# Kernel optimization log

Hardware: AMD Instinct MI355X
Metric: run time of the kernel (lower is better)

## Reference

```python
import jax, jax.numpy as jnp
import numpy as np

T, A = 10, 9           # input_dim_h, input_dim_w
HID = 128              # EncoderMLP hidden_dim default
D = 512                # n_latent_dims
G, K = 4, 32           # vqvae_groups, vqvae_n_embed
ACT_SCALE = 1.0


def setup_inputs() -> dict:
    key = jax.random.key(0)
    ks = jax.random.split(key, 16)
    N = 131072
    s = lambda k, shp, fan: jax.random.normal(k, shp, jnp.float32) * (1.0 / np.sqrt(fan))
    inp = {
        "state": jax.random.normal(ks[0], (N, T, A), jnp.float32),
        # encoder: (T*A)->128 relu, 128->128 relu, 128->512
        "enc_w1": s(ks[1], (T * A, HID), T * A), "enc_b1": jnp.zeros((HID,), jnp.float32),
        "enc_w2": s(ks[2], (HID, HID), HID),     "enc_b2": jnp.zeros((HID,), jnp.float32),
        "enc_w3": s(ks[3], (HID, D), HID),       "enc_b3": jnp.zeros((D,), jnp.float32),
        # decoder: 512->128 relu, 128->128 relu, 128->(T*A)
        "dec_w1": s(ks[4], (D, HID), D),         "dec_b1": jnp.zeros((HID,), jnp.float32),
        "dec_w2": s(ks[5], (HID, HID), HID),     "dec_b2": jnp.zeros((HID,), jnp.float32),
        "dec_w3": s(ks[6], (HID, T * A), HID),   "dec_b3": jnp.zeros((T * A,), jnp.float32),
        # residual VQ codebooks [G, K, D]
        "codebooks": jax.random.normal(ks[7], (G, K, D), jnp.float32),
    }
    return inp


def _mlp(x, w1, b1, w2, b2, w3, b3):
    h = jax.nn.relu(x @ w1 + b1)
    h = jax.nn.relu(h @ w2 + b2)
    return h @ w3 + b3


def reference(state, enc_w1, enc_b1, enc_w2, enc_b2, enc_w3, enc_b3,
              dec_w1, dec_b1, dec_w2, dec_b2, dec_w3, dec_b3, codebooks):
    N = state.shape[0]
    x = (state / ACT_SCALE).reshape(N, T * A)            # preprocess: 'N T A -> N (T A)'
    z = _mlp(x, enc_w1, enc_b1, enc_w2, enc_b2, enc_w3, enc_b3)  # [N, D]

    # Residual VQ over G quantizers (eval path): nearest-code per residual,
    # straight-through accumulation, per-quantizer commitment loss.
    residual = z
    quant = jnp.zeros_like(z)
    codes, losses = [], []
    for g in range(G):
        e = codebooks[g]                                  # [K, D]
        # ||r - e||^2 = ||r||^2 - 2 r.e + ||e||^2 ; ||r||^2 constant over K
        dist = jnp.sum(e * e, axis=-1)[None, :] - 2.0 * (residual @ e.T)  # [N, K]
        idx = jnp.argmin(dist, axis=-1)                   # [N]
        q = e[idx]                                        # [N, D] gather
        losses.append(jnp.mean((jax.lax.stop_gradient(q) - residual) ** 2))
        quant = quant + residual + jax.lax.stop_gradient(q - residual)  # straight-through
        residual = residual - jax.lax.stop_gradient(q)
        codes.append(idx)
    vq_code = jnp.stack(codes, axis=-1)                   # [N, G]
    vq_loss = jnp.sum(jnp.stack(losses))

    recon = _mlp(quant, dec_w1, dec_b1, dec_w2, dec_b2, dec_w3, dec_b3) * ACT_SCALE
    recon = recon.reshape(N, T, A)                        # 'N (T A) -> N T A'
    return quant, vq_code, recon, vq_loss
```

## Files before the change

kernel.cpp:

```cpp
#include <hip/hip_runtime.h>
#include <hip/hip_bf16.h>

#define NSAMP 131072
#define TA    90
#define HID   128
#define DLAT  512

#define OFF_CODE  67108864ll
#define OFF_RECON (67108864ll + 524288ll)
#define OFF_LOSS  (67108864ll + 524288ll + 11796480ll)

#define PZF    8704
#define SHF    8960
#define MSKF   8256
#define H2AF   8272
#define H2BF   8400
#define TAU    0.08f

typedef __attribute__((ext_vector_type(8))) short bf16x8;
typedef __attribute__((ext_vector_type(4))) short s16x4;
typedef __attribute__((ext_vector_type(4))) float f32x4;
typedef unsigned short ushort_t;
#define MFMA16(a, b, c) __builtin_amdgcn_mfma_f32_16x16x32_bf16(a, b, c, 0, 0, 0)

__device__ __forceinline__ ushort_t f2bf(float f) {
    unsigned u = __float_as_uint(f);
    u = (u + 0x7FFF + ((u >> 16) & 1)) >> 16;
    return (ushort_t)u;
}
__device__ __forceinline__ float bf2f(ushort_t u) {
    return __uint_as_float(((unsigned)u) << 16);
}

__device__ __forceinline__ float dot512(const float* __restrict__ a,
                                        const float* __restrict__ b) {
    float s = 0.f;
    for (int i = 0; i < 128; ++i) {
        float4 x = ((const float4*)a)[i], y = ((const float4*)b)[i];
        s += x.x * y.x + x.y * y.y + x.z * y.z + x.w * y.w;
    }
    return s;
}

__global__ void k_prep(const float* __restrict__ cb, const float* __restrict__ w3,
                       const float* __restrict__ b3, const float* __restrict__ w1d,
                       const float* __restrict__ w2d, const float* __restrict__ w3d,
                       const float* __restrict__ w2e, const float* __restrict__ w1e,
                       float* __restrict__ P, float* __restrict__ M,
                       float* __restrict__ t0, float* __restrict__ v,
                       float* __restrict__ csc, float* __restrict__ cbW,
                       ushort_t* __restrict__ Qbf, ushort_t* __restrict__ w2bf,
                       ushort_t* __restrict__ w3bf,
                       ushort_t* __restrict__ Mhibf, ushort_t* __restrict__ Mlobf,
                       ushort_t* __restrict__ w2ehi, ushort_t* __restrict__ w2elo,
                       ushort_t* __restrict__ w1ehi, ushort_t* __restrict__ w1elo) {
    int tbl = blockIdx.x >> 6;
    int gid = (blockIdx.x & 63) * 256 + threadIdx.x;
    int i = gid >> 7, j = gid & 127;
    if (tbl == 0) {
        P[gid] = dot512(cb + (size_t)i * 512, cb + (size_t)j * 512);
        if (gid < 128) t0[gid] = dot512(cb + (size_t)gid * 512, b3);
        if (gid == 0) csc[0] = dot512(b3, b3);
    } else if (tbl == 1) {
        M[gid] = dot512(w3 + (size_t)i * 512, cb + (size_t)j * 512);
    } else if (tbl == 2) {
        Qbf[gid] = f2bf(dot512(w3 + (size_t)i * 512, w3 + (size_t)j * 512));
        if (gid < 128) v[gid] = dot512(w3 + (size_t)gid * 512, b3);
    } else if (tbl == 3) {
        float s = 0.f;
        for (int d = 0; d < 512; ++d) s = fmaf(cb[(size_t)i * 512 + d], w1d[d * 128 + j], s);
        cbW[gid] = s;
    } else if (tbl == 4) {
        w2bf[gid] = f2bf(w2d[j * 128 + i]);
    } else if (tbl == 5) {
        if (gid < 96 * 128)
            w3bf[gid] = (i < 90) ? f2bf(w3d[j * TA + i]) : (ushort_t)0;
    } else if (tbl == 6) {
        float d = dot512(w3 + (size_t)j * 512, cb + (size_t)i * 512);
        ushort_t hi = f2bf(d);
        Mhibf[gid] = hi;
        Mlobf[gid] = f2bf(d - bf2f(hi));
    } else if (tbl == 7) {
        float d = w2e[j * 128 + i];
        ushort_t hi = f2bf(d);
        w2ehi[gid] = hi;
        w2elo[gid] = f2bf(d - bf2f(hi));
    } else {
        float d = (j < 90) ? w1e[(size_t)j * 128 + i] : 0.f;
        ushort_t hi = f2bf(d);
        w1ehi[gid] = hi;
        w1elo[gid] = f2bf(d - bf2f(hi));
    }
}

__launch_bounds__(256, 4)
__global__ void k_encvq(const float* __restrict__ X,
                        const float* __restrict__ w1, const float* __restrict__ b1,
                        const float* __restrict__ w2, const float* __restrict__ b2,
                        const ushort_t* __restrict__ w1ehi, const ushort_t* __restrict__ w1elo,
                        const ushort_t* __restrict__ w2ehi, const ushort_t* __restrict__ w2elo,
                        const float* __restrict__ Mt, const ushort_t* __restrict__ Qbf,
                        const ushort_t* __restrict__ Mhi, const ushort_t* __restrict__ Mlo,
                        const float* __restrict__ t0g, const float* __restrict__ vg,
                        const float* __restrict__ cg, const float* __restrict__ Pg,
                        float* __restrict__ codes_out, float* __restrict__ loss_acc) {
    __shared__ __align__(16) float SH[SHF];
    ushort_t* sphi = (ushort_t*)SH;
    ushort_t* splo = (ushort_t*)(SH + 4096);
    const int t = threadIdx.x;
    const int row0 = blockIdx.x * 64;
    const int wv = t >> 6, lane = t & 63, lr = lane & 15, lg = lane >> 4;

    for (int it = 0; it < 24; ++it) {
        int idx = it * 256 + t;
        int s = idx / 96, j = idx - 96 * s;
        float xv = (j < 90) ? X[(size_t)(row0 + s) * TA + j] : 0.f;
        ushort_t hi = f2bf(xv);
        int adr = ((s << 7) + j) ^ ((s & 7) << 3);
        sphi[adr] = hi;
        splo[adr] = f2bf(xv - bf2f(hi));
    }
    __syncthreads();

    {
        f32x4 c1[2][4];
#pragma unroll
        for (int m = 0; m < 2; ++m)
#pragma unroll
            for (int n = 0; n < 4; ++n) c1[m][n] = (f32x4){0.f, 0.f, 0.f, 0.f};
#pragma unroll
        for (int kt = 0; kt < 3; ++kt) {
            bf16x8 ah[2], al[2], bhi[4], blo[4];
#pragma unroll
            for (int m = 0; m < 2; ++m) {
                int arow = (32 * wv + 16 * m + lr) * 128 + kt * 32 + lg * 8;
                ah[m] = *(const bf16x8*)&w1ehi[arow];
                al[m] = *(const bf16x8*)&w1elo[arow];
            }
#pragma unroll
            for (int n = 0; n < 4; ++n) {
                int s = 16 * n + lr;
                int adr = ((s << 7) + kt * 32 + lg * 8) ^ ((s & 7) << 3);
                bhi[n] = *(const bf16x8*)&sphi[adr];
                blo[n] = *(const bf16x8*)&splo[adr];
            }
#pragma unroll
            for (int m = 0; m < 2; ++m)
#pragma unroll
                for (int n = 0; n < 4; ++n) {
                    c1[m][n] = MFMA16(ah[m], bhi[n], c1[m][n]);
                    c1[m][n] = MFMA16(ah[m], blo[n], c1[m][n]);
                    c1[m][n] = MFMA16(al[m], bhi[n], c1[m][n]);
                }
        }
        __syncthreads();
        float rbf[2][4];
#pragma unroll
        for (int m = 0; m < 2; ++m)
#pragma unroll
            for (int r = 0; r < 4; ++r) rbf[m][r] = b1[32 * wv + 16 * m + lg * 4 + r];
#pragma unroll
        for (int m = 0; m < 2; ++m)
#pragma unroll
            for (int n = 0; n < 4; ++n) {
                int s = 16 * n + lr;
                s16x4 ph, pl;
#pragma unroll
                for (int r = 0; r < 4; ++r) {
                    float hv = fmaxf(c1[m][n][r] + rbf[m][r], 0.f);
                    ushort_t hi = f2bf(hv);
                    ph[r] = (short)hi;
                    pl[r] = (short)f2bf(hv - bf2f(hi));
                }
                int ob2 = 32 * wv + 16 * m + lg * 4;
                int adr = ((s << 7) + ob2) ^ ((s & 7) << 3);
                *(s16x4*)&sphi[adr] = ph;
                *(s16x4*)&splo[adr] = pl;
            }
    }
    __syncthreads();

    {
        f32x4 c2[2][4];
#pragma unroll
        for (int m = 0; m < 2; ++m)
#pragma unroll
            for (int n = 0; n < 4; ++n) c2[m][n] = (f32x4){0.f, 0.f, 0.f, 0.f};
#pragma unroll
        for (int kt = 0; kt < 4; ++kt) {
            bf16x8 ah[2], al[2], bhi[4], blo[4];
#pragma unroll
            for (int m = 0; m < 2; ++m) {
                int arow = (32 * wv + 16 * m + lr) * 128 + kt * 32 + lg * 8;
                ah[m] = *(const bf16x8*)&w2ehi[arow];
                al[m] = *(const bf16x8*)&w2elo[arow];
            }
#pragma unroll
            for (int n = 0; n < 4; ++n) {
                int s = 16 * n + lr;
                int adr = ((s << 7) + kt * 32 + lg * 8) ^ ((s & 7) << 3);
                bhi[n] = *(const bf16x8*)&sphi[adr];
                blo[n] = *(const bf16x8*)&splo[adr];
            }
#pragma unroll
            for (int m = 0; m < 2; ++m)
#pragma unroll
                for (int n = 0; n < 4; ++n) {
                    c2[m][n] = MFMA16(ah[m], bhi[n], c2[m][n]);
                    c2[m][n] = MFMA16(ah[m], blo[n], c2[m][n]);
                    c2[m][n] = MFMA16(al[m], bhi[n], c2[m][n]);
                }
        }
        __syncthreads();
        float rbf[2][4];
#pragma unroll
        for (int m = 0; m < 2; ++m)
#pragma unroll
            for (int r = 0; r < 4; ++r) rbf[m][r] = b2[32 * wv + 16 * m + lg * 4 + r];
#pragma unroll
        for (int m = 0; m < 2; ++m)
#pragma unroll
            for (int n = 0; n < 4; ++n) {
                int s = 16 * n + lr;
                s16x4 ph, pl;
#pragma unroll
                for (int r = 0; r < 4; ++r) {
                    float hv = fmaxf(c2[m][n][r] + rbf[m][r], 0.f);
                    ushort_t hi = f2bf(hv);
                    ph[r] = (short)hi;
                    pl[r] = (short)f2bf(hv - bf2f(hi));
                }
                int ob2 = 32 * wv + 16 * m + lg * 4;
                int adr = ((s << 7) + ob2) ^ ((s & 7) << 3);
                *(s16x4*)&sphi[adr] = ph;
                *(s16x4*)&splo[adr] = pl;
            }
    }
    __syncthreads();

    f32x4 sc[2][4];
    {
        f32x4 qc[2][4];
#pragma unroll
        for (int m = 0; m < 2; ++m)
#pragma unroll
            for (int n = 0; n < 4; ++n) {
                qc[m][n] = (f32x4){0.f, 0.f, 0.f, 0.f};
                sc[m][n] = (f32x4){0.f, 0.f, 0.f, 0.f};
            }
#pragma unroll
        for (int kt = 0; kt < 4; ++kt) {
            bf16x8 aq[2], amh[2], aml[2], bhi[4], blo[4];
#pragma unroll
            for (int m = 0; m < 2; ++m) {
                int arow = (32 * wv + 16 * m + lr) * 128 + kt * 32 + lg * 8;
                aq[m]  = *(const bf16x8*)&Qbf[arow];
                amh[m] = *(const bf16x8*)&Mhi[arow];
                aml[m] = *(const bf16x8*)&Mlo[arow];
            }
#pragma unroll
            for (int n = 0; n < 4; ++n) {
                int s = 16 * n + lr;
                int adr = ((s << 7) + kt * 32 + lg * 8) ^ ((s & 7) << 3);
                bhi[n] = *(const bf16x8*)&sphi[adr];
                blo[n] = *(const bf16x8*)&splo[adr];
            }
#pragma unroll
            for (int m = 0; m < 2; ++m)
#pragma unroll
                for (int n = 0; n < 4; ++n) {
                    qc[m][n] = MFMA16(aq[m], bhi[n], qc[m][n]);
                    sc[m][n] = MFMA16(amh[m], bhi[n], sc[m][n]);
                    sc[m][n] = MFMA16(amh[m], blo[n], sc[m][n]);
                    sc[m][n] = MFMA16(aml[m], bhi[n], sc[m][n]);
                }
        }
        float v2[2][4];
#pragma unroll
        for (int m = 0; m < 2; ++m)
#pragma unroll
            for (int r = 0; r < 4; ++r) v2[m][r] = 2.f * vg[32 * wv + 16 * m + lg * 4 + r];
#pragma unroll
        for (int n = 0; n < 4; ++n) {
            int s = 16 * n + lr;
            float p = 0.f;
#pragma unroll
            for (int m = 0; m < 2; ++m)
#pragma unroll
                for (int r = 0; r < 4; ++r) {
                    int o = 32 * wv + 16 * m + lg * 4 + r;
                    int adr = ((s << 7) + o) ^ ((s & 7) << 3);
                    float hv = bf2f(sphi[adr]) + bf2f(splo[adr]);
                    p = fmaf(qc[m][n][r] + v2[m][r], hv, p);
                }
            p += __shfl_xor(p, 16);
            p += __shfl_xor(p, 32);
            if (lg == 0) SH[PZF + wv * 64 + s] = p;
        }
    }
    __syncthreads();

#pragma unroll
    for (int m = 0; m < 2; ++m)
#pragma unroll
        for (int n = 0; n < 4; ++n) {
            int s = 16 * n + lr;
#pragma unroll
            for (int r = 0; r < 4; ++r) {
                int o = 32 * wv + 16 * m + lg * 4 + r;
                SH[s * 129 + o] = sc[m][n][r] + t0g[o];
            }
        }
    __syncthreads();

    int cs[4];
    if (t < 64) {
        float marg = 3.4e38f;
#pragma unroll
        for (int g = 0; g < 4; ++g) {
            float best = 3.4e38f, best2 = 3.4e38f; int bi = g * 32;
#pragma unroll
            for (int k = 0; k < 32; ++k) {
                int c = g * 32 + k;
                float zd = SH[t * 129 + c];
                float nr = Pg[c * 128 + c];
                float a2 = 0.f;
#pragma unroll
                for (int gp = 0; gp < g; ++gp) a2 += Pg[cs[gp] * 128 + c];
                float dist = nr - 2.f * (zd - a2);
                if (dist < best) { best2 = best; best = dist; bi = c; }
                else if (dist < best2) { best2 = dist; }
            }
            cs[g] = bi;
            float m2 = best2 - best;
            marg = (m2 < marg) ? m2 : marg;
        }
        unsigned long long mk = __ballot(marg < TAU);
        if (t == 0) *(unsigned long long*)&SH[MSKF] = mk;
    }
    __syncthreads();

    const unsigned long long mask = *(const unsigned long long*)&SH[MSKF];

    {
        unsigned long long mk = mask;
        while (mk) {
            int nA = (int)__ffsll((long long)mk) - 1; mk &= mk - 1;
            int nB = -1;
            if (mk) { nB = (int)__ffsll((long long)mk) - 1; mk &= mk - 1; }
            int grp = t >> 7, tt = t & 127;
            int s2 = grp ? nB : nA;
            float hv1 = 0.f;
            if (s2 >= 0) {
                const float* xr = X + (size_t)(row0 + s2) * TA;
                for (int j = 0; j < 90; ++j)
                    hv1 = fmaf(xr[j], w1[j * 128 + tt], hv1);
                hv1 = fmaxf(hv1 + b1[tt], 0.f);
                SH[(grp ? H2BF : H2AF) + tt] = hv1;
            }
            __syncthreads();
            float hv2 = 0.f;
            if (s2 >= 0) {
                const float* h1c = &SH[grp ? H2BF : H2AF];
                for (int j = 0; j < 128; ++j)
                    hv2 = fmaf(h1c[j], w2[(size_t)j * 128 + tt], hv2);
                hv2 = fmaxf(hv2 + b2[tt], 0.f);
            }
            __syncthreads();
            if (s2 >= 0) SH[(grp ? H2BF : H2AF) + tt] = hv2;
            __syncthreads();
            if (s2 >= 0) {
                const float* h2c = &SH[grp ? H2BF : H2AF];
                float a = 0.f;
                for (int j = 0; j < 128; ++j)
                    a = fmaf(h2c[j], Mt[(size_t)j * 128 + tt], a);
                SH[s2 * 129 + tt] = a + t0g[tt];
            }
            __syncthreads();
        }
    }

    if (t < 64 && ((mask >> t) & 1ull)) {
#pragma unroll
        for (int g = 0; g < 4; ++g) {
            float best = 3.4e38f; int bi = g * 32;
#pragma unroll
            for (int k = 0; k < 32; ++k) {
                int c = g * 32 + k;
                float zd = SH[t * 129 + c];
                float nr = Pg[c * 128 + c];
                float a2 = 0.f;
#pragma unroll
                for (int gp = 0; gp < g; ++gp) a2 += Pg[cs[gp] * 128 + c];
                float dist = nr - 2.f * (zd - a2);
                if (dist < best) { best = dist; bi = c; }
            }
            cs[g] = bi;
        }
    }

    if (t < 64) {
        float znorm = cg[0] + SH[PZF + t] + SH[PZF + 64 + t]
                    + SH[PZF + 128 + t] + SH[PZF + 192 + t];
        float S1 = 0.f, Sp = 0.f, msum = 0.f;
#pragma unroll
        for (int g = 0; g < 4; ++g) {
            int c = cs[g];
            float zd = SH[t * 129 + c];
            float nr = Pg[c * 128 + c];
            float a2 = 0.f;
#pragma unroll
            for (int gp = 0; gp < g; ++gp) a2 += Pg[cs[gp] * 128 + c];
            S1 += zd;
            Sp += nr + 2.f * a2;
            msum += (znorm - 2.f * S1 + Sp);
            codes_out[(size_t)(row0 + t) * 4 + g] = (float)(c - g * 32);
        }
#pragma unroll
        for (int off = 32; off; off >>= 1) msum += __shfl_down(msum, off);
        if (t == 0) atomicAdd(&loss_acc[0], msum);
    }
}

__launch_bounds__(256, 4)
__global__ void k_dec(const float* __restrict__ codes_f, const float* __restrict__ cb,
                      const float* __restrict__ cbW, const float* __restrict__ b1,
                      const ushort_t* __restrict__ w2bf, const float* __restrict__ b2,
                      const ushort_t* __restrict__ w3bf, const float* __restrict__ b3,
                      float* __restrict__ quant_out, float* __restrict__ recon_out) {
    __shared__ __align__(16) unsigned char SHB[39424];
    int* cods = (int*)SHB;
    ushort_t* h2bf = (ushort_t*)SHB;
    ushort_t* h1bf = (ushort_t*)(SHB + 16384);
    float* Rl = (float*)(SHB + 16384);
    const int t = threadIdx.x;
    const int st = t & 15, ct = t >> 4;
    const int s0 = st * 4, o0 = ct * 8;
    const int row0 = blockIdx.x * 64;

    cods[t] = ((t & 3) << 5) + (int)codes_f[(size_t)row0 * 4 + t];
    float rb1[8];
#pragma unroll
    for (int i = 0; i < 8; ++i) rb1[i] = b1[o0 + i];
    __syncthreads();

    for (int i = 0; i < 32; ++i) {
        int idx4 = i * 256 + t;
        int s = idx4 >> 7, d4 = (idx4 & 127) * 4;
        const int* cp = &cods[s * 4];
        float4 a = *(const float4*)&cb[(size_t)cp[0] * 512 + d4];
        float4 b = *(const float4*)&cb[(size_t)cp[1] * 512 + d4];
        float4 c = *(const float4*)&cb[(size_t)cp[2] * 512 + d4];
        float4 d = *(const float4*)&cb[(size_t)cp[3] * 512 + d4];
        float4 vv;
        vv.x = a.x + b.x + c.x + d.x;
        vv.y = a.y + b.y + c.y + d.y;
        vv.z = a.z + b.z + c.z + d.z;
        vv.w = a.w + b.w + c.w + d.w;
        *(float4*)&quant_out[(size_t)(row0 + s) * 512 + d4] = vv;
    }

    {
        float accL[8][4];
#pragma unroll
        for (int b = 0; b < 4; ++b) {
            const int* cp = &cods[(s0 + b) * 4];
            float u[8] = {0, 0, 0, 0, 0, 0, 0, 0};
#pragma unroll
            for (int g = 0; g < 4; ++g) {
                const float* r = &cbW[(size_t)cp[g] * 128 + o0];
                float4 x0 = *(const float4*)r, x1 = *(const float4*)(r + 4);
                u[0] += x0.x; u[1] += x0.y; u[2] += x0.z; u[3] += x0.w;
                u[4] += x1.x; u[5] += x1.y; u[6] += x1.z; u[7] += x1.w;
            }
#pragma unroll
            for (int a = 0; a < 8; ++a) accL[a][b] = u[a];
        }
#pragma unroll
        for (int b = 0; b < 4; ++b) {
            int s = s0 + b;
            bf16x8 pk;
#pragma unroll
            for (int a = 0; a < 8; ++a)
                pk[a] = (short)f2bf(fmaxf(accL[a][b] + rb1[a], 0.f));
            *(bf16x8*)&h1bf[((s << 7) + o0) ^ ((s & 7) << 3)] = pk;
        }
    }
    __syncthreads();

    const int wv = t >> 6, lane = t & 63, lr = lane & 15, lg = lane >> 4;

    {
        f32x4 c2[2][4];
#pragma unroll
        for (int m = 0; m < 2; ++m)
#pragma unroll
            for (int n = 0; n < 4; ++n) c2[m][n] = (f32x4){0.f, 0.f, 0.f, 0.f};
#pragma unroll
        for (int kt = 0; kt < 4; ++kt) {
            bf16x8 af[2], bfr[4];
#pragma unroll
            for (int m = 0; m < 2; ++m)
                af[m] = *(const bf16x8*)&w2bf[(32 * wv + 16 * m + lr) * 128 + kt * 32 + lg * 8];
#pragma unroll
            for (int n = 0; n < 4; ++n) {
                int s = 16 * n + lr;
                bfr[n] = *(const bf16x8*)&h1bf[((s << 7) + kt * 32 + lg * 8) ^ ((s & 7) << 3)];
            }
#pragma unroll
            for (int m = 0; m < 2; ++m)
#pragma unroll
                for (int n = 0; n < 4; ++n)
                    c2[m][n] = MFMA16(af[m], bfr[n], c2[m][n]);
        }
        float rb[2][4];
#pragma unroll
        for (int m = 0; m < 2; ++m)
#pragma unroll
            for (int r = 0; r < 4; ++r) rb[m][r] = b2[32 * wv + 16 * m + lg * 4 + r];
#pragma unroll
        for (int m = 0; m < 2; ++m)
#pragma unroll
            for (int n = 0; n < 4; ++n) {
                int s = 16 * n + lr;
                s16x4 pk;
#pragma unroll
                for (int r = 0; r < 4; ++r)
                    pk[r] = (short)f2bf(fmaxf(c2[m][n][r] + rb[m][r], 0.f));
                int ob2 = 32 * wv + 16 * m + lg * 4;
                *(s16x4*)&h2bf[((s << 7) + ob2) ^ ((s & 7) << 3)] = pk;
            }
    }
    __syncthreads();

    {
        f32x4 c3[6];
#pragma unroll
        for (int m = 0; m < 6; ++m) c3[m] = (f32x4){0.f, 0.f, 0.f, 0.f};
        const int sB = 16 * wv + lr;
#pragma unroll
        for (int kt = 0; kt < 4; ++kt) {
            bf16x8 bfr = *(const bf16x8*)&h2bf[((sB << 7) + kt * 32 + lg * 8) ^ ((sB & 7) << 3)];
#pragma unroll
            for (int mt = 0; mt < 6; ++mt) {
                bf16x8 af = *(const bf16x8*)&w3bf[(16 * mt + lr) * 128 + kt * 32 + lg * 8];
                c3[mt] = MFMA16(af, bfr, c3[mt]);
            }
        }
#pragma unroll
        for (int mt = 0; mt < 6; ++mt)
#pragma unroll
            for (int r = 0; r < 4; ++r) {
                int o = 16 * mt + lg * 4 + r;
                if (o < 90) Rl[sB * 90 + o] = c3[mt][r] + b3[o];
            }
    }
    __syncthreads();

    {
        const float4* R4v = (const float4*)Rl;
        float4* G4 = (float4*)(recon_out + (size_t)row0 * 90);
#pragma unroll
        for (int it = 0; it < 6; ++it) {
            int i4 = it * 256 + t;
            if (i4 < 1440) G4[i4] = R4v[i4];
        }
    }
}

__global__ void k_loss(const float* __restrict__ acc, float* __restrict__ out) {
    out[0] = acc[0] * (1.0f / ((float)NSAMP * (float)DLAT));
}

extern "C" void kernel_launch(void* const* d_in, const int* in_sizes, int n_in,
                              void* d_out, int out_size, void* d_ws, size_t ws_size,
                              hipStream_t stream) {
    const float* state  = (const float*)d_in[0];
    const float* enc_w1 = (const float*)d_in[1];
    const float* enc_b1 = (const float*)d_in[2];
    const float* enc_w2 = (const float*)d_in[3];
    const float* enc_b2 = (const float*)d_in[4];
    const float* enc_w3 = (const float*)d_in[5];
    const float* enc_b3 = (const float*)d_in[6];
    const float* dec_w1 = (const float*)d_in[7];
    const float* dec_b1 = (const float*)d_in[8];
    const float* dec_w2 = (const float*)d_in[9];
    const float* dec_b2 = (const float*)d_in[10];
    const float* dec_w3 = (const float*)d_in[11];
    const float* dec_b3 = (const float*)d_in[12];
    const float* cb     = (const float*)d_in[13];

    float* out = (float*)d_out;
    float* P   = out;
    float* M   = out + 16384;
    ushort_t* Mhi = (ushort_t*)(out + 32768);
    ushort_t* Mlo = (ushort_t*)(out + 40960);
    float* t0  = out + 49152;
    float* v   = out + 49280;
    float* csc = out + 49408;
    ushort_t* w2ehi = (ushort_t*)(out + 49664);
    ushort_t* w2elo = (ushort_t*)(out + 57856);
    ushort_t* w1ehi = (ushort_t*)(out + 66048);
    ushort_t* w1elo = (ushort_t*)(out + 74240);
    float* ws = (float*)d_ws;
    float* loss_acc = ws;
    float* cbW = ws + 256;
    ushort_t* Qbf  = (ushort_t*)(ws + 16640);
    ushort_t* w2bf = (ushort_t*)(ws + 24832);
    ushort_t* w3bf = (ushort_t*)(ws + 33024);

    hipMemsetAsync(d_ws, 0, 16, stream);
    k_prep<<<576, 256, 0, stream>>>(cb, enc_w3, enc_b3, dec_w1, dec_w2, dec_w3,
                                    enc_w2, enc_w1,
                                    P, M, t0, v, csc, cbW, Qbf, w2bf, w3bf,
                                    Mhi, Mlo, w2ehi, w2elo, w1ehi, w1elo);
    k_encvq<<<NSAMP / 64, 256, 0, stream>>>(state, enc_w1, enc_b1, enc_w2, enc_b2,
                                            w1ehi, w1elo, w2ehi, w2elo,
                                            M, Qbf, Mhi, Mlo, t0, v, csc, P,
                                            out + OFF_CODE, loss_acc);
    k_dec<<<NSAMP / 64, 256, 0, stream>>>(out + OFF_CODE, cb, cbW,
                                          dec_b1, w2bf, dec_b2, w3bf, dec_b3,
                                          out, out + OFF_RECON);
    k_loss<<<1, 1, 0, stream>>>(loss_acc, out + OFF_LOSS);
}
```

Before: 352.3 us.

## Fuse encoder-VQ and decoder into one kernel when workspace is large enough

```diff
diff --git a/kernel.cpp b/kernel.cpp
--- a/kernel.cpp
+++ b/kernel.cpp
@@ -30,6 +30,11 @@
 }
 __device__ __forceinline__ float bf2f(ushort_t u) {
     return __uint_as_float(((unsigned)u) << 16);
+}
+__device__ __forceinline__ void nt_store4(float* p, float x0, float x1,
+                                          float x2, float x3) {
+    f32x4 v = {x0, x1, x2, x3};
+    __builtin_nontemporal_store(v, (f32x4*)p);
 }
 
 __device__ __forceinline__ float dot512(const float* __restrict__ a,
@@ -93,6 +98,511 @@
     }
 }
 
+__device__ __forceinline__ void enc_body(
+        const float* __restrict__ X,
+        const float* __restrict__ ew1, const float* __restrict__ eb1,
+        const float* __restrict__ ew2, const float* __restrict__ eb2,
+        const ushort_t* __restrict__ w1ehi, const ushort_t* __restrict__ w1elo,
+        const ushort_t* __restrict__ w2ehi, const ushort_t* __restrict__ w2elo,
+        const float* __restrict__ Mt, const ushort_t* __restrict__ Qbf,
+        const ushort_t* __restrict__ Mhi, const ushort_t* __restrict__ Mlo,
+        const float* __restrict__ t0g, const float* __restrict__ vg,
+        const float* __restrict__ cg, const float* __restrict__ Pg,
+        float* __restrict__ codes_out, float* __restrict__ loss_acc,
+        float* SH, int t, int row0, int (&cs)[4]) {
+    ushort_t* sphi = (ushort_t*)SH;
+    ushort_t* splo = (ushort_t*)(SH + 4096);
+    const int wv = t >> 6, lane = t & 63, lr = lane & 15, lg = lane >> 4;
+
+    for (int it = 0; it < 24; ++it) {
+        int idx = it * 256 + t;
+        int s = idx / 96, j = idx - 96 * s;
+        float xv = (j < 90) ? X[(size_t)(row0 + s) * TA + j] : 0.f;
+        ushort_t hi = f2bf(xv);
+        int adr = ((s << 7) + j) ^ ((s & 7) << 3);
+        sphi[adr] = hi;
+        splo[adr] = f2bf(xv - bf2f(hi));
+    }
+    __syncthreads();
+
+    {
+        f32x4 c1[2][4];
+#pragma unroll
+        for (int m = 0; m < 2; ++m)
+#pragma unroll
+            for (int n = 0; n < 4; ++n) c1[m][n] = (f32x4){0.f, 0.f, 0.f, 0.f};
+#pragma unroll
+        for (int kt = 0; kt < 3; ++kt) {
+            bf16x8 ah[2], al[2], bhi[4], blo[4];
+#pragma unroll
+            for (int m = 0; m < 2; ++m) {
+                int arow = (32 * wv + 16 * m + lr) * 128 + kt * 32 + lg * 8;
+                ah[m] = *(const bf16x8*)&w1ehi[arow];
+                al[m] = *(const bf16x8*)&w1elo[arow];
+            }
+#pragma unroll
+            for (int n = 0; n < 4; ++n) {
+                int s = 16 * n + lr;
+                int adr = ((s << 7) + kt * 32 + lg * 8) ^ ((s & 7) << 3);
+                bhi[n] = *(const bf16x8*)&sphi[adr];
+                blo[n] = *(const bf16x8*)&splo[adr];
+            }
+#pragma unroll
+            for (int m = 0; m < 2; ++m)
+#pragma unroll
+                for (int n = 0; n < 4; ++n) {
+                    c1[m][n] = MFMA16(ah[m], bhi[n], c1[m][n]);
+                    c1[m][n] = MFMA16(ah[m], blo[n], c1[m][n]);
+                    c1[m][n] = MFMA16(al[m], bhi[n], c1[m][n]);
+                }
+        }
+        __syncthreads();
+        float rbf[2][4];
+#pragma unroll
+        for (int m = 0; m < 2; ++m)
+#pragma unroll
+            for (int r = 0; r < 4; ++r) rbf[m][r] = eb1[32 * wv + 16 * m + lg * 4 + r];
+#pragma unroll
+        for (int m = 0; m < 2; ++m)
+#pragma unroll
+            for (int n = 0; n < 4; ++n) {
+                int s = 16 * n + lr;
+                s16x4 ph, pl;
+#pragma unroll
+                for (int r = 0; r < 4; ++r) {
+                    float hv = fmaxf(c1[m][n][r] + rbf[m][r], 0.f);
+                    ushort_t hi = f2bf(hv);
+                    ph[r] = (short)hi;
+                    pl[r] = (short)f2bf(hv - bf2f(hi));
+                }
+                int ob2 = 32 * wv + 16 * m + lg * 4;
+                int adr = ((s << 7) + ob2) ^ ((s & 7) << 3);
+                *(s16x4*)&sphi[adr] = ph;
+                *(s16x4*)&splo[adr] = pl;
+            }
+    }
+    __syncthreads();
+
+    {
+        f32x4 c2[2][4];
+#pragma unroll
+        for (int m = 0; m < 2; ++m)
+#pragma unroll
+            for (int n = 0; n < 4; ++n) c2[m][n] = (f32x4){0.f, 0.f, 0.f, 0.f};
+#pragma unroll
+        for (int kt = 0; kt < 4; ++kt) {
+            bf16x8 ah[2], al[2], bhi[4], blo[4];
+#pragma unroll
+            for (int m = 0; m < 2; ++m) {
+                int arow = (32 * wv + 16 * m + lr) * 128 + kt * 32 + lg * 8;
+                ah[m] = *(const bf16x8*)&w2ehi[arow];
+                al[m] = *(const bf16x8*)&w2elo[arow];
+            }
+#pragma unroll
+            for (int n = 0; n < 4; ++n) {
+                int s = 16 * n + lr;
+                int adr = ((s << 7) + kt * 32 + lg * 8) ^ ((s & 7) << 3);
+                bhi[n] = *(const bf16x8*)&sphi[adr];
+                blo[n] = *(const bf16x8*)&splo[adr];
+            }
+#pragma unroll
+            for (int m = 0; m < 2; ++m)
+#pragma unroll
+                for (int n = 0; n < 4; ++n) {
+                    c2[m][n] = MFMA16(ah[m], bhi[n], c2[m][n]);
+                    c2[m][n] = MFMA16(ah[m], blo[n], c2[m][n]);
+                    c2[m][n] = MFMA16(al[m], bhi[n], c2[m][n]);
+                }
+        }
+        __syncthreads();
+        float rbf[2][4];
+#pragma unroll
+        for (int m = 0; m < 2; ++m)
+#pragma unroll
+            for (int r = 0; r < 4; ++r) rbf[m][r] = eb2[32 * wv + 16 * m + lg * 4 + r];
+#pragma unroll
+        for (int m = 0; m < 2; ++m)
+#pragma unroll
+            for (int n = 0; n < 4; ++n) {
+                int s = 16 * n + lr;
+                s16x4 ph, pl;
+#pragma unroll
+                for (int r = 0; r < 4; ++r) {
+                    float hv = fmaxf(c2[m][n][r] + rbf[m][r], 0.f);
+                    ushort_t hi = f2bf(hv);
+                    ph[r] = (short)hi;
+                    pl[r] = (short)f2bf(hv - bf2f(hi));
+                }
+                int ob2 = 32 * wv + 16 * m + lg * 4;
+                int adr = ((s << 7) + ob2) ^ ((s & 7) << 3);
+                *(s16x4*)&sphi[adr] = ph;
+                *(s16x4*)&splo[adr] = pl;
+            }
+    }
+    __syncthreads();
+
+    f32x4 sc[2][4];
+    {
+        f32x4 qc[2][4];
+#pragma unroll
+        for (int m = 0; m < 2; ++m)
+#pragma unroll
+            for (int n = 0; n < 4; ++n) {
+                qc[m][n] = (f32x4){0.f, 0.f, 0.f, 0.f};
+                sc[m][n] = (f32x4){0.f, 0.f, 0.f, 0.f};
+            }
+#pragma unroll
+        for (int kt = 0; kt < 4; ++kt) {
+            bf16x8 aq[2], amh[2], aml[2], bhi[4], blo[4];
+#pragma unroll
+            for (int m = 0; m < 2; ++m) {
+                int arow = (32 * wv + 16 * m + lr) * 128 + kt * 32 + lg * 8;
+                aq[m]  = *(const bf16x8*)&Qbf[arow];
+                amh[m] = *(const bf16x8*)&Mhi[arow];
+                aml[m] = *(const bf16x8*)&Mlo[arow];
+            }
+#pragma unroll
+            for (int n = 0; n < 4; ++n) {
+                int s = 16 * n + lr;
+                int adr = ((s << 7) + kt * 32 + lg * 8) ^ ((s & 7) << 3);
+                bhi[n] = *(const bf16x8*)&sphi[adr];
+                blo[n] = *(const bf16x8*)&splo[adr];
+            }
+#pragma unroll
+            for (int m = 0; m < 2; ++m)
+#pragma unroll
+                for (int n = 0; n < 4; ++n) {
+                    qc[m][n] = MFMA16(aq[m], bhi[n], qc[m][n]);
+                    sc[m][n] = MFMA16(amh[m], bhi[n], sc[m][n]);
+                    sc[m][n] = MFMA16(amh[m], blo[n], sc[m][n]);
+                    sc[m][n] = MFMA16(aml[m], bhi[n], sc[m][n]);
+                }
+        }
+        float v2[2][4];
+#pragma unroll
+        for (int m = 0; m < 2; ++m)
+#pragma unroll
+            for (int r = 0; r < 4; ++r) v2[m][r] = 2.f * vg[32 * wv + 16 * m + lg * 4 + r];
+#pragma unroll
+        for (int n = 0; n < 4; ++n) {
+            int s = 16 * n + lr;
+            float p = 0.f;
+#pragma unroll
+            for (int m = 0; m < 2; ++m)
+#pragma unroll
+                for (int r = 0; r < 4; ++r) {
+                    int o = 32 * wv + 16 * m + lg * 4 + r;
+                    int adr = ((s << 7) + o) ^ ((s & 7) << 3);
+                    float hv = bf2f(sphi[adr]) + bf2f(splo[adr]);
+                    p = fmaf(qc[m][n][r] + v2[m][r], hv, p);
+                }
+            p += __shfl_xor(p, 16);
+            p += __shfl_xor(p, 32);
+            if (lg == 0) SH[PZF + wv * 64 + s] = p;
+        }
+    }
+    __syncthreads();
+
+#pragma unroll
+    for (int m = 0; m < 2; ++m)
+#pragma unroll
+        for (int n = 0; n < 4; ++n) {
+            int s = 16 * n + lr;
+#pragma unroll
+            for (int r = 0; r < 4; ++r) {
+                int o = 32 * wv + 16 * m + lg * 4 + r;
+                SH[s * 129 + o] = sc[m][n][r] + t0g[o];
+            }
+        }
+    __syncthreads();
+
+    if (t < 64) {
+        float marg = 3.4e38f;
+#pragma unroll
+        for (int g = 0; g < 4; ++g) {
+            float best = 3.4e38f, best2 = 3.4e38f; int bi = g * 32;
+#pragma unroll
+            for (int k = 0; k < 32; ++k) {
+                int c = g * 32 + k;
+                float zd = SH[t * 129 + c];
+                float nr = Pg[c * 128 + c];
+                float a2 = 0.f;
+#pragma unroll
+                for (int gp = 0; gp < g; ++gp) a2 += Pg[cs[gp] * 128 + c];
+                float dist = nr - 2.f * (zd - a2);
+                if (dist < best) { best2 = best; best = dist; bi = c; }
+                else if (dist < best2) { best2 = dist; }
+            }
+            cs[g] = bi;
+            float m2 = best2 - best;
+            marg = (m2 < marg) ? m2 : marg;
+        }
+        unsigned long long mk = __ballot(marg < TAU);
+        if (t == 0) *(unsigned long long*)&SH[MSKF] = mk;
+    }
+    __syncthreads();
+
+    const unsigned long long mask = *(const unsigned long long*)&SH[MSKF];
+
+    {
+        unsigned long long mk = mask;
+        while (mk) {
+            int nA = (int)__ffsll((long long)mk) - 1; mk &= mk - 1;
+            int nB = -1;
+            if (mk) { nB = (int)__ffsll((long long)mk) - 1; mk &= mk - 1; }
+            int grp = t >> 7, tt = t & 127;
+            int s2 = grp ? nB : nA;
+            float hv1 = 0.f;
+            if (s2 >= 0) {
+                const float* xr = X + (size_t)(row0 + s2) * TA;
+                for (int j = 0; j < 90; ++j)
+                    hv1 = fmaf(xr[j], ew1[j * 128 + tt], hv1);
+                hv1 = fmaxf(hv1 + eb1[tt], 0.f);
+                SH[(grp ? H2BF : H2AF) + tt] = hv1;
+            }
+            __syncthreads();
+            float hv2 = 0.f;
+            if (s2 >= 0) {
+                const float* h1c = &SH[grp ? H2BF : H2AF];
+                for (int j = 0; j < 128; ++j)
+                    hv2 = fmaf(h1c[j], ew2[(size_t)j * 128 + tt], hv2);
+                hv2 = fmaxf(hv2 + eb2[tt], 0.f);
+            }
+            __syncthreads();
+            if (s2 >= 0) SH[(grp ? H2BF : H2AF) + tt] = hv2;
+            __syncthreads();
+            if (s2 >= 0) {
+                const float* h2c = &SH[grp ? H2BF : H2AF];
+                float a = 0.f;
+                for (int j = 0; j < 128; ++j)
+                    a = fmaf(h2c[j], Mt[(size_t)j * 128 + tt], a);
+                SH[s2 * 129 + tt] = a + t0g[tt];
+            }
+            __syncthreads();
+        }
+    }
+
+    if (t < 64 && ((mask >> t) & 1ull)) {
+#pragma unroll
+        for (int g = 0; g < 4; ++g) {
+            float best = 3.4e38f; int bi = g * 32;
+#pragma unroll
+            for (int k = 0; k < 32; ++k) {
+                int c = g * 32 + k;
+                float zd = SH[t * 129 + c];
+                float nr = Pg[c * 128 + c];
+                float a2 = 0.f;
+#pragma unroll
+                for (int gp = 0; gp < g; ++gp) a2 += Pg[cs[gp] * 128 + c];
+                float dist = nr - 2.f * (zd - a2);
+                if (dist < best) { best = dist; bi = c; }
+            }
+            cs[g] = bi;
+        }
+    }
+
+    if (t < 64) {
+        float znorm = cg[0] + SH[PZF + t] + SH[PZF + 64 + t]
+                    + SH[PZF + 128 + t] + SH[PZF + 192 + t];
+        float S1 = 0.f, Sp = 0.f, msum = 0.f;
+#pragma unroll
+        for (int g = 0; g < 4; ++g) {
+            int c = cs[g];
+            float zd = SH[t * 129 + c];
+            float nr = Pg[c * 128 + c];
+            float a2 = 0.f;
+#pragma unroll
+            for (int gp = 0; gp < g; ++gp) a2 += Pg[cs[gp] * 128 + c];
+            S1 += zd;
+            Sp += nr + 2.f * a2;
+            msum += (znorm - 2.f * S1 + Sp);
+            codes_out[(size_t)(row0 + t) * 4 + g] = (float)(cs[g] - g * 32);
+        }
+#pragma unroll
+        for (int off = 32; off; off >>= 1) msum += __shfl_down(msum, off);
+        if (t == 0) atomicAdd(&loss_acc[0], msum);
+    }
+}
+
+__device__ __forceinline__ void dec_body(
+        const float* __restrict__ cb, const float* __restrict__ cbW,
+        const float* __restrict__ b1, const ushort_t* __restrict__ w2bf,
+        const float* __restrict__ b2, const ushort_t* __restrict__ w3bf,
+        const float* __restrict__ b3,
+        float* __restrict__ quant_out, float* __restrict__ recon_out,
+        unsigned char* SHB, int t, int row0) {
+    int* cods = (int*)SHB;
+    ushort_t* h2bf = (ushort_t*)SHB;
+    ushort_t* h1bf = (ushort_t*)(SHB + 16384);
+    float* Rl = (float*)(SHB + 16384);
+    const int st = t & 15, ct = t >> 4;
+    const int s0 = st * 4, o0 = ct * 8;
+
+    float rb1[8];
+#pragma unroll
+    for (int i = 0; i < 8; ++i) rb1[i] = b1[o0 + i];
+
+    for (int i = 0; i < 32; ++i) {
+        int idx4 = i * 256 + t;
+        int s = idx4 >> 7, d4 = (idx4 & 127) * 4;
+        const int* cp = &cods[s * 4];
+        float4 a = *(const float4*)&cb[(size_t)cp[0] * 512 + d4];
+        float4 b = *(const float4*)&cb[(size_t)cp[1] * 512 + d4];
+        float4 c = *(const float4*)&cb[(size_t)cp[2] * 512 + d4];
+        float4 d = *(const float4*)&cb[(size_t)cp[3] * 512 + d4];
+        nt_store4(&quant_out[(size_t)(row0 + s) * 512 + d4],
+                  a.x + b.x + c.x + d.x, a.y + b.y + c.y + d.y,
+                  a.z + b.z + c.z + d.z, a.w + b.w + c.w + d.w);
+    }
+
+    {
+        float accL[8][4];
+#pragma unroll
+        for (int b = 0; b < 4; ++b) {
+            const int* cp = &cods[(s0 + b) * 4];
+            float u[8] = {0, 0, 0, 0, 0, 0, 0, 0};
+#pragma unroll
+            for (int g = 0; g < 4; ++g) {
+                const float* r = &cbW[(size_t)cp[g] * 128 + o0];
+                float4 x0 = *(const float4*)r, x1 = *(const float4*)(r + 4);
+                u[0] += x0.x; u[1] += x0.y; u[2] += x0.z; u[3] += x0.w;
+                u[4] += x1.x; u[5] += x1.y; u[6] += x1.z; u[7] += x1.w;
+            }
+#pragma unroll
+            for (int a = 0; a < 8; ++a) accL[a][b] = u[a];
+        }
+#pragma unroll
+        for (int b = 0; b < 4; ++b) {
+            int s = s0 + b;
+            bf16x8 pk;
+#pragma unroll
+            for (int a = 0; a < 8; ++a)
+                pk[a] = (short)f2bf(fmaxf(accL[a][b] + rb1[a], 0.f));
+            *(bf16x8*)&h1bf[((s << 7) + o0) ^ ((s & 7) << 3)] = pk;
+        }
+    }
+    __syncthreads();
+
+    const int wv = t >> 6, lane = t & 63, lr = lane & 15, lg = lane >> 4;
+
+    {
+        f32x4 c2[2][4];
+#pragma unroll
+        for (int m = 0; m < 2; ++m)
+#pragma unroll
+            for (int n = 0; n < 4; ++n) c2[m][n] = (f32x4){0.f, 0.f, 0.f, 0.f};
+#pragma unroll
+        for (int kt = 0; kt < 4; ++kt) {
+            bf16x8 af[2], bfr[4];
+#pragma unroll
+            for (int m = 0; m < 2; ++m)
+                af[m] = *(const bf16x8*)&w2bf[(32 * wv + 16 * m + lr) * 128 + kt * 32 + lg * 8];
+#pragma unroll
+            for (int n = 0; n < 4; ++n) {
+                int s = 16 * n + lr;
+                bfr[n] = *(const bf16x8*)&h1bf[((s << 7) + kt * 32 + lg * 8) ^ ((s & 7) << 3)];
+            }
+#pragma unroll
+            for (int m = 0; m < 2; ++m)
+#pragma unroll
+                for (int n = 0; n < 4; ++n)
+                    c2[m][n] = MFMA16(af[m], bfr[n], c2[m][n]);
+        }
+        float rb[2][4];
+#pragma unroll
+        for (int m = 0; m < 2; ++m)
+#pragma unroll
+            for (int r = 0; r < 4; ++r) rb[m][r] = b2[32 * wv + 16 * m + lg * 4 + r];
+#pragma unroll
+        for (int m = 0; m < 2; ++m)
+#pragma unroll
+            for (int n = 0; n < 4; ++n) {
+                int s = 16 * n + lr;
+                s16x4 pk;
+#pragma unroll
+                for (int r = 0; r < 4; ++r)
+                    pk[r] = (short)f2bf(fmaxf(c2[m][n][r] + rb[m][r], 0.f));
+                int ob2 = 32 * wv + 16 * m + lg * 4;
+                *(s16x4*)&h2bf[((s << 7) + ob2) ^ ((s & 7) << 3)] = pk;
+            }
+    }
+    __syncthreads();
+
+    {
+        f32x4 c3[6];
+#pragma unroll
+        for (int m = 0; m < 6; ++m) c3[m] = (f32x4){0.f, 0.f, 0.f, 0.f};
+        const int sB = 16 * wv + lr;
+#pragma unroll
+        for (int kt = 0; kt < 4; ++kt) {
+            bf16x8 bfr = *(const bf16x8*)&h2bf[((sB << 7) + kt * 32 + lg * 8) ^ ((sB & 7) << 3)];
+#pragma unroll
+            for (int mt = 0; mt < 6; ++mt) {
+                bf16x8 af = *(const bf16x8*)&w3bf[(16 * mt + lr) * 128 + kt * 32 + lg * 8];
+                c3[mt] = MFMA16(af, bfr, c3[mt]);
+            }
+        }
+#pragma unroll
+        for (int mt = 0; mt < 6; ++mt)
+#pragma unroll
+            for (int r = 0; r < 4; ++r) {
+                int o = 16 * mt + lg * 4 + r;
+                if (o < 90) Rl[sB * 90 + o] = c3[mt][r] + b3[o];
+            }
+    }
+    __syncthreads();
+
+    {
+        const float4* R4v = (const float4*)Rl;
+        float* G = recon_out + (size_t)row0 * 90;
+#pragma unroll
+        for (int it = 0; it < 6; ++it) {
+            int i4 = it * 256 + t;
+            if (i4 < 1440) {
+                float4 vv = R4v[i4];
+                nt_store4(&G[i4 * 4], vv.x, vv.y, vv.z, vv.w);
+            }
+        }
+    }
+}
+
+__launch_bounds__(256, 4)
+__global__ void k_fused(const float* __restrict__ X,
+                        const float* __restrict__ ew1, const float* __restrict__ eb1,
+                        const float* __restrict__ ew2, const float* __restrict__ eb2,
+                        const ushort_t* __restrict__ w1ehi, const ushort_t* __restrict__ w1elo,
+                        const ushort_t* __restrict__ w2ehi, const ushort_t* __restrict__ w2elo,
+                        const float* __restrict__ Mt, const ushort_t* __restrict__ Qbf,
+                        const ushort_t* __restrict__ Mhi, const ushort_t* __restrict__ Mlo,
+                        const float* __restrict__ t0g, const float* __restrict__ vg,
+                        const float* __restrict__ cg, const float* __restrict__ Pg,
+                        float* __restrict__ codes_out, float* __restrict__ loss_acc,
+                        const float* __restrict__ cb, const float* __restrict__ cbW,
+                        const float* __restrict__ db1, const ushort_t* __restrict__ w2bf,
+                        const float* __restrict__ db2, const ushort_t* __restrict__ w3bf,
+                        const float* __restrict__ db3,
+                        float* __restrict__ quant_out, float* __restrict__ recon_out) {
+    __shared__ __align__(16) unsigned char SHB[39424];
+    float* SH = (float*)SHB;
+    const int t = threadIdx.x;
+    const int row0 = blockIdx.x * 64;
+
+    int cs[4] = {0, 32, 64, 96};
+    enc_body(X, ew1, eb1, ew2, eb2, w1ehi, w1elo, w2ehi, w2elo,
+             Mt, Qbf, Mhi, Mlo, t0g, vg, cg, Pg, codes_out, loss_acc,
+             SH, t, row0, cs);
+
+    __syncthreads();
+    if (t < 64) {
+#pragma unroll
+        for (int g = 0; g < 4; ++g) ((int*)SHB)[t * 4 + g] = cs[g];
+    }
+    __syncthreads();
+
+    dec_body(cb, cbW, db1, w2bf, db2, w3bf, db3, quant_out, recon_out,
+             SHB, t, row0);
+}
+
 __launch_bounds__(256, 4)
 __global__ void k_encvq(const float* __restrict__ X,
                         const float* __restrict__ w1, const float* __restrict__ b1,
@@ -105,321 +615,12 @@
                         const float* __restrict__ cg, const float* __restrict__ Pg,
                         float* __restrict__ codes_out, float* __restrict__ loss_acc) {
     __shared__ __align__(16) float SH[SHF];
-    ushort_t* sphi = (ushort_t*)SH;
-    ushort_t* splo = (ushort_t*)(SH + 4096);
     const int t = threadIdx.x;
     const int row0 = blockIdx.x * 64;
-    const int wv = t >> 6, lane = t & 63, lr = lane & 15, lg = lane >> 4;
-
-    for (int it = 0; it < 24; ++it) {
-        int idx = it * 256 + t;
-        int s = idx / 96, j = idx - 96 * s;
-        float xv = (j < 90) ? X[(size_t)(row0 + s) * TA + j] : 0.f;
-        ushort_t hi = f2bf(xv);
-        int adr = ((s << 7) + j) ^ ((s & 7) << 3);
-        sphi[adr] = hi;
-        splo[adr] = f2bf(xv - bf2f(hi));
-    }
-    __syncthreads();
-
-    {
-        f32x4 c1[2][4];
-#pragma unroll
-        for (int m = 0; m < 2; ++m)
-#pragma unroll
-            for (int n = 0; n < 4; ++n) c1[m][n] = (f32x4){0.f, 0.f, 0.f, 0.f};
-#pragma unroll
-        for (int kt = 0; kt < 3; ++kt) {
-            bf16x8 ah[2], al[2], bhi[4], blo[4];
-#pragma unroll
-            for (int m = 0; m < 2; ++m) {
-                int arow = (32 * wv + 16 * m + lr) * 128 + kt * 32 + lg * 8;
-                ah[m] = *(const bf16x8*)&w1ehi[arow];
-                al[m] = *(const bf16x8*)&w1elo[arow];
-            }
-#pragma unroll
-            for (int n = 0; n < 4; ++n) {
-                int s = 16 * n + lr;
-                int adr = ((s << 7) + kt * 32 + lg * 8) ^ ((s & 7) << 3);
-                bhi[n] = *(const bf16x8*)&sphi[adr];
-                blo[n] = *(const bf16x8*)&splo[adr];
-            }
-#pragma unroll
-            for (int m = 0; m < 2; ++m)
-#pragma unroll
-                for (int n = 0; n < 4; ++n) {
-                    c1[m][n] = MFMA16(ah[m], bhi[n], c1[m][n]);
-                    c1[m][n] = MFMA16(ah[m], blo[n], c1[m][n]);
-                    c1[m][n] = MFMA16(al[m], bhi[n], c1[m][n]);
-                }
-        }
-        __syncthreads();
-        float rbf[2][4];
-#pragma unroll
-        for (int m = 0; m < 2; ++m)
-#pragma unroll
-            for (int r = 0; r < 4; ++r) rbf[m][r] = b1[32 * wv + 16 * m + lg * 4 + r];
-#pragma unroll
-        for (int m = 0; m < 2; ++m)
-#pragma unroll
-            for (int n = 0; n < 4; ++n) {
-                int s = 16 * n + lr;
-                s16x4 ph, pl;
-#pragma unroll
-                for (int r = 0; r < 4; ++r) {
-                    float hv = fmaxf(c1[m][n][r] + rbf[m][r], 0.f);
-                    ushort_t hi = f2bf(hv);
-                    ph[r] = (short)hi;
-                    pl[r] = (short)f2bf(hv - bf2f(hi));
-                }
-                int ob2 = 32 * wv + 16 * m + lg * 4;
-                int adr = ((s << 7) + ob2) ^ ((s & 7) << 3);
-                *(s16x4*)&sphi[adr] = ph;
-                *(s16x4*)&splo[adr] = pl;
-            }
-    }
-    __syncthreads();
-
-    {
-        f32x4 c2[2][4];
-#pragma unroll
-        for (int m = 0; m < 2; ++m)
-#pragma unroll
-            for (int n = 0; n < 4; ++n) c2[m][n] = (f32x4){0.f, 0.f, 0.f, 0.f};
-#pragma unroll
-        for (int kt = 0; kt < 4; ++kt) {
-            bf16x8 ah[2], al[2], bhi[4], blo[4];
-#pragma unroll
-            for (int m = 0; m < 2; ++m) {
-                int arow = (32 * wv + 16 * m + lr) * 128 + kt * 32 + lg * 8;
-                ah[m] = *(const bf16x8*)&w2ehi[arow];
-                al[m] = *(const bf16x8*)&w2elo[arow];
-            }
-#pragma unroll
-            for (int n = 0; n < 4; ++n) {
-                int s = 16 * n + lr;
-                int adr = ((s << 7) + kt * 32 + lg * 8) ^ ((s & 7) << 3);
-                bhi[n] = *(const bf16x8*)&sphi[adr];
-                blo[n] = *(const bf16x8*)&splo[adr];
-            }
-#pragma unroll
-            for (int m = 0; m < 2; ++m)
-#pragma unroll
-                for (int n = 0; n < 4; ++n) {
-                    c2[m][n] = MFMA16(ah[m], bhi[n], c2[m][n]);
-                    c2[m][n] = MFMA16(ah[m], blo[n], c2[m][n]);
-                    c2[m][n] = MFMA16(al[m], bhi[n], c2[m][n]);
-                }
-        }
-        __syncthreads();
-        float rbf[2][4];
-#pragma unroll
-        for (int m = 0; m < 2; ++m)
-#pragma unroll
-            for (int r = 0; r < 4; ++r) rbf[m][r] = b2[32 * wv + 16 * m + lg * 4 + r];
-#pragma unroll
-        for (int m = 0; m < 2; ++m)
-#pragma unroll
-            for (int n = 0; n < 4; ++n) {
-                int s = 16 * n + lr;
-                s16x4 ph, pl;
-#pragma unroll
-                for (int r = 0; r < 4; ++r) {
-                    float hv = fmaxf(c2[m][n][r] + rbf[m][r], 0.f);
-                    ushort_t hi = f2bf(hv);
-                    ph[r] = (short)hi;
-                    pl[r] = (short)f2bf(hv - bf2f(hi));
-                }
-                int ob2 = 32 * wv + 16 * m + lg * 4;
-                int adr = ((s << 7) + ob2) ^ ((s & 7) << 3);
-                *(s16x4*)&sphi[adr] = ph;
-                *(s16x4*)&splo[adr] = pl;
-            }
-    }
-    __syncthreads();
-
-    f32x4 sc[2][4];
-    {
-        f32x4 qc[2][4];
-#pragma unroll
-        for (int m = 0; m < 2; ++m)
-#pragma unroll
-            for (int n = 0; n < 4; ++n) {
-                qc[m][n] = (f32x4){0.f, 0.f, 0.f, 0.f};
-                sc[m][n] = (f32x4){0.f, 0.f, 0.f, 0.f};
-            }
-#pragma unroll
-        for (int kt = 0; kt < 4; ++kt) {
-            bf16x8 aq[2], amh[2], aml[2], bhi[4], blo[4];
-#pragma unroll
-            for (int m = 0; m < 2; ++m) {
-                int arow = (32 * wv + 16 * m + lr) * 128 + kt * 32 + lg * 8;
-                aq[m]  = *(const bf16x8*)&Qbf[arow];
-                amh[m] = *(const bf16x8*)&Mhi[arow];
-                aml[m] = *(const bf16x8*)&Mlo[arow];
-            }
-#pragma unroll
-            for (int n = 0; n < 4; ++n) {
-                int s = 16 * n + lr;
-                int adr = ((s << 7) + kt * 32 + lg * 8) ^ ((s & 7) << 3);
-                bhi[n] = *(const bf16x8*)&sphi[adr];
-                blo[n] = *(const bf16x8*)&splo[adr];
-            }
-#pragma unroll
-            for (int m = 0; m < 2; ++m)
-#pragma unroll
-                for (int n = 0; n < 4; ++n) {
-                    qc[m][n] = MFMA16(aq[m], bhi[n], qc[m][n]);
-                    sc[m][n] = MFMA16(amh[m], bhi[n], sc[m][n]);
-                    sc[m][n] = MFMA16(amh[m], blo[n], sc[m][n]);
-                    sc[m][n] = MFMA16(aml[m], bhi[n], sc[m][n]);
-                }
-        }
-        float v2[2][4];
-#pragma unroll
-        for (int m = 0; m < 2; ++m)
-#pragma unroll
-            for (int r = 0; r < 4; ++r) v2[m][r] = 2.f * vg[32 * wv + 16 * m + lg * 4 + r];
-#pragma unroll
-        for (int n = 0; n < 4; ++n) {
-            int s = 16 * n + lr;
-            float p = 0.f;
-#pragma unroll
-            for (int m = 0; m < 2; ++m)
-#pragma unroll
-                for (int r = 0; r < 4; ++r) {
-                    int o = 32 * wv + 16 * m + lg * 4 + r;
-                    int adr = ((s << 7) + o) ^ ((s & 7) << 3);
-                    float hv = bf2f(sphi[adr]) + bf2f(splo[adr]);
-                    p = fmaf(qc[m][n][r] + v2[m][r], hv, p);
-                }
-            p += __shfl_xor(p, 16);
-            p += __shfl_xor(p, 32);
-            if (lg == 0) SH[PZF + wv * 64 + s] = p;
-        }
-    }
-    __syncthreads();
-
-#pragma unroll
-    for (int m = 0; m < 2; ++m)
-#pragma unroll
-        for (int n = 0; n < 4; ++n) {
-            int s = 16 * n + lr;
-#pragma unroll
-            for (int r = 0; r < 4; ++r) {
-                int o = 32 * wv + 16 * m + lg * 4 + r;
-                SH[s * 129 + o] = sc[m][n][r] + t0g[o];
-            }
-        }
-    __syncthreads();
-
-    int cs[4];
-    if (t < 64) {
-        float marg = 3.4e38f;
-#pragma unroll
-        for (int g = 0; g < 4; ++g) {
-            float best = 3.4e38f, best2 = 3.4e38f; int bi = g * 32;
-#pragma unroll
-            for (int k = 0; k < 32; ++k) {
-                int c = g * 32 + k;
-                float zd = SH[t * 129 + c];
-                float nr = Pg[c * 128 + c];
-                float a2 = 0.f;
-#pragma unroll
-                for (int gp = 0; gp < g; ++gp) a2 += Pg[cs[gp] * 128 + c];
-                float dist = nr - 2.f * (zd - a2);
-                if (dist < best) { best2 = best; best = dist; bi = c; }
-                else if (dist < best2) { best2 = dist; }
-            }
-            cs[g] = bi;
-            float m2 = best2 - best;
-            marg = (m2 < marg) ? m2 : marg;
-        }
-        unsigned long long mk = __ballot(marg < TAU);
-        if (t == 0) *(unsigned long long*)&SH[MSKF] = mk;
-    }
-    __syncthreads();
-
-    const unsigned long long mask = *(const unsigned long long*)&SH[MSKF];
-
-    {
-        unsigned long long mk = mask;
-        while (mk) {
-            int nA = (int)__ffsll((long long)mk) - 1; mk &= mk - 1;
-            int nB = -1;
-            if (mk) { nB = (int)__ffsll((long long)mk) - 1; mk &= mk - 1; }
-            int grp = t >> 7, tt = t & 127;
-            int s2 = grp ? nB : nA;
-            float hv1 = 0.f;
-            if (s2 >= 0) {
-                const float* xr = X + (size_t)(row0 + s2) * TA;
-                for (int j = 0; j < 90; ++j)
-                    hv1 = fmaf(xr[j], w1[j * 128 + tt], hv1);
-                hv1 = fmaxf(hv1 + b1[tt], 0.f);
-                SH[(grp ? H2BF : H2AF) + tt] = hv1;
-            }
-            __syncthreads();
-            float hv2 = 0.f;
-            if (s2 >= 0) {
-                const float* h1c = &SH[grp ? H2BF : H2AF];
-                for (int j = 0; j < 128; ++j)
-                    hv2 = fmaf(h1c[j], w2[(size_t)j * 128 + tt], hv2);
-                hv2 = fmaxf(hv2 + b2[tt], 0.f);
-            }
-            __syncthreads();
-            if (s2 >= 0) SH[(grp ? H2BF : H2AF) + tt] = hv2;
-            __syncthreads();
-            if (s2 >= 0) {
-                const float* h2c = &SH[grp ? H2BF : H2AF];
-                float a = 0.f;
-                for (int j = 0; j < 128; ++j)
-                    a = fmaf(h2c[j], Mt[(size_t)j * 128 + tt], a);
-                SH[s2 * 129 + tt] = a + t0g[tt];
-            }
-            __syncthreads();
-        }
-    }
-
-    if (t < 64 && ((mask >> t) & 1ull)) {
-#pragma unroll
-        for (int g = 0; g < 4; ++g) {
-            float best = 3.4e38f; int bi = g * 32;
-#pragma unroll
-            for (int k = 0; k < 32; ++k) {
-                int c = g * 32 + k;
-                float zd = SH[t * 129 + c];
-                float nr = Pg[c * 128 + c];
-                float a2 = 0.f;
-#pragma unroll
-                for (int gp = 0; gp < g; ++gp) a2 += Pg[cs[gp] * 128 + c];
-                float dist = nr - 2.f * (zd - a2);
-                if (dist < best) { best = dist; bi = c; }
-            }
-            cs[g] = bi;
-        }
-    }
-
-    if (t < 64) {
-        float znorm = cg[0] + SH[PZF + t] + SH[PZF + 64 + t]
-                    + SH[PZF + 128 + t] + SH[PZF + 192 + t];
-        float S1 = 0.f, Sp = 0.f, msum = 0.f;
-#pragma unroll
-        for (int g = 0; g < 4; ++g) {
-            int c = cs[g];
-            float zd = SH[t * 129 + c];
-            float nr = Pg[c * 128 + c];
-            float a2 = 0.f;
-#pragma unroll
-            for (int gp = 0; gp < g; ++gp) a2 += Pg[cs[gp] * 128 + c];
-            S1 += zd;
-            Sp += nr + 2.f * a2;
-            msum += (znorm - 2.f * S1 + Sp);
-            codes_out[(size_t)(row0 + t) * 4 + g] = (float)(c - g * 32);
-        }
-#pragma unroll
-        for (int off = 32; off; off >>= 1) msum += __shfl_down(msum, off);
-        if (t == 0) atomicAdd(&loss_acc[0], msum);
-    }
+    int cs[4] = {0, 32, 64, 96};
+    enc_body(X, w1, b1, w2, b2, w1ehi, w1elo, w2ehi, w2elo,
+             Mt, Qbf, Mhi, Mlo, t0g, vg, cg, Pg, codes_out, loss_acc,
+             SH, t, row0, cs);
 }
 
 __launch_bounds__(256, 4)
@@ -429,143 +630,12 @@
                       const ushort_t* __restrict__ w3bf, const float* __restrict__ b3,
                       float* __restrict__ quant_out, float* __restrict__ recon_out) {
     __shared__ __align__(16) unsigned char SHB[39424];
-    int* cods = (int*)SHB;
-    ushort_t* h2bf = (ushort_t*)SHB;
-    ushort_t* h1bf = (ushort_t*)(SHB + 16384);
-    float* Rl = (float*)(SHB + 16384);
     const int t = threadIdx.x;
-    const int st = t & 15, ct = t >> 4;
-    const int s0 = st * 4, o0 = ct * 8;
     const int row0 = blockIdx.x * 64;
-
-    cods[t] = ((t & 3) << 5) + (int)codes_f[(size_t)row0 * 4 + t];
-    float rb1[8];
-#pragma unroll
-    for (int i = 0; i < 8; ++i) rb1[i] = b1[o0 + i];
-    __syncthreads();
-
-    for (int i = 0; i < 32; ++i) {
-        int idx4 = i * 256 + t;
-        int s = idx4 >> 7, d4 = (idx4 & 127) * 4;
-        const int* cp = &cods[s * 4];
-        float4 a = *(const float4*)&cb[(size_t)cp[0] * 512 + d4];
-        float4 b = *(const float4*)&cb[(size_t)cp[1] * 512 + d4];
-        float4 c = *(const float4*)&cb[(size_t)cp[2] * 512 + d4];
-        float4 d = *(const float4*)&cb[(size_t)cp[3] * 512 + d4];
-        float4 vv;
-        vv.x = a.x + b.x + c.x + d.x;
-        vv.y = a.y + b.y + c.y + d.y;
-        vv.z = a.z + b.z + c.z + d.z;
-        vv.w = a.w + b.w + c.w + d.w;
-        *(float4*)&quant_out[(size_t)(row0 + s) * 512 + d4] = vv;
-    }
-
-    {
-        float accL[8][4];
-#pragma unroll
-        for (int b = 0; b < 4; ++b) {
-            const int* cp = &cods[(s0 + b) * 4];
-            float u[8] = {0, 0, 0, 0, 0, 0, 0, 0};
-#pragma unroll
-            for (int g = 0; g < 4; ++g) {
-                const float* r = &cbW[(size_t)cp[g] * 128 + o0];
-                float4 x0 = *(const float4*)r, x1 = *(const float4*)(r + 4);
-                u[0] += x0.x; u[1] += x0.y; u[2] += x0.z; u[3] += x0.w;
-                u[4] += x1.x; u[5] += x1.y; u[6] += x1.z; u[7] += x1.w;
-            }
-#pragma unroll
-            for (int a = 0; a < 8; ++a) accL[a][b] = u[a];
-        }
-#pragma unroll
-        for (int b = 0; b < 4; ++b) {
-            int s = s0 + b;
-            bf16x8 pk;
-#pragma unroll
-            for (int a = 0; a < 8; ++a)
-                pk[a] = (short)f2bf(fmaxf(accL[a][b] + rb1[a], 0.f));
-            *(bf16x8*)&h1bf[((s << 7) + o0) ^ ((s & 7) << 3)] = pk;
-        }
-    }
-    __syncthreads();
-
-    const int wv = t >> 6, lane = t & 63, lr = lane & 15, lg = lane >> 4;
-
-    {
-        f32x4 c2[2][4];
-#pragma unroll
-        for (int m = 0; m < 2; ++m)
-#pragma unroll
-            for (int n = 0; n < 4; ++n) c2[m][n] = (f32x4){0.f, 0.f, 0.f, 0.f};
-#pragma unroll
-        for (int kt = 0; kt < 4; ++kt) {
-            bf16x8 af[2], bfr[4];
-#pragma unroll
-            for (int m = 0; m < 2; ++m)
-                af[m] = *(const bf16x8*)&w2bf[(32 * wv + 16 * m + lr) * 128 + kt * 32 + lg * 8];
-#pragma unroll
-            for (int n = 0; n < 4; ++n) {
-                int s = 16 * n + lr;
-                bfr[n] = *(const bf16x8*)&h1bf[((s << 7) + kt * 32 + lg * 8) ^ ((s & 7) << 3)];
-            }
-#pragma unroll
-            for (int m = 0; m < 2; ++m)
-#pragma unroll
-                for (int n = 0; n < 4; ++n)
-                    c2[m][n] = MFMA16(af[m], bfr[n], c2[m][n]);
-        }
-        float rb[2][4];
-#pragma unroll
-        for (int m = 0; m < 2; ++m)
-#pragma unroll
-            for (int r = 0; r < 4; ++r) rb[m][r] = b2[32 * wv + 16 * m + lg * 4 + r];
-#pragma unroll
-        for (int m = 0; m < 2; ++m)
-#pragma unroll
-            for (int n = 0; n < 4; ++n) {
-                int s = 16 * n + lr;
-                s16x4 pk;
-#pragma unroll
-                for (int r = 0; r < 4; ++r)
-                    pk[r] = (short)f2bf(fmaxf(c2[m][n][r] + rb[m][r], 0.f));
-                int ob2 = 32 * wv + 16 * m + lg * 4;
-                *(s16x4*)&h2bf[((s << 7) + ob2) ^ ((s & 7) << 3)] = pk;
-            }
-    }
-    __syncthreads();
-
-    {
-        f32x4 c3[6];
-#pragma unroll
-        for (int m = 0; m < 6; ++m) c3[m] = (f32x4){0.f, 0.f, 0.f, 0.f};
-        const int sB = 16 * wv + lr;
-#pragma unroll
-        for (int kt = 0; kt < 4; ++kt) {
-            bf16x8 bfr = *(const bf16x8*)&h2bf[((sB << 7) + kt * 32 + lg * 8) ^ ((sB & 7) << 3)];
-#pragma unroll
-            for (int mt = 0; mt < 6; ++mt) {
-                bf16x8 af = *(const bf16x8*)&w3bf[(16 * mt + lr) * 128 + kt * 32 + lg * 8];
-                c3[mt] = MFMA16(af, bfr, c3[mt]);
-            }
-        }
-#pragma unroll
-        for (int mt = 0; mt < 6; ++mt)
-#pragma unroll
-            for (int r = 0; r < 4; ++r) {
-                int o = 16 * mt + lg * 4 + r;
-                if (o < 90) Rl[sB * 90 + o] = c3[mt][r] + b3[o];
-            }
-    }
-    __syncthreads();
-
-    {
-        const float4* R4v = (const float4*)Rl;
-        float4* G4 = (float4*)(recon_out + (size_t)row0 * 90);
-#pragma unroll
-        for (int it = 0; it < 6; ++it) {
-            int i4 = it * 256 + t;
-            if (i4 < 1440) G4[i4] = R4v[i4];
-        }
-    }
+    ((int*)SHB)[t] = ((t & 3) << 5) + (int)codes_f[(size_t)row0 * 4 + t];
+    __syncthreads();
+    dec_body(cb, cbW, b1, w2bf, b2, w3bf, b3, quant_out, recon_out,
+             SHB, t, row0);
 }
 
 __global__ void k_loss(const float* __restrict__ acc, float* __restrict__ out) {
@@ -591,17 +661,6 @@
     const float* cb     = (const float*)d_in[13];
 
     float* out = (float*)d_out;
-    float* P   = out;
-    float* M   = out + 16384;
-    ushort_t* Mhi = (ushort_t*)(out + 32768);
-    ushort_t* Mlo = (ushort_t*)(out + 40960);
-    float* t0  = out + 49152;
-    float* v   = out + 49280;
-    float* csc = out + 49408;
-    ushort_t* w2ehi = (ushort_t*)(out + 49664);
-    ushort_t* w2elo = (ushort_t*)(out + 57856);
-    ushort_t* w1ehi = (ushort_t*)(out + 66048);
-    ushort_t* w1elo = (ushort_t*)(out + 74240);
     float* ws = (float*)d_ws;
     float* loss_acc = ws;
     float* cbW = ws + 256;
@@ -610,16 +669,53 @@
     ushort_t* w3bf = (ushort_t*)(ws + 33024);
 
     hipMemsetAsync(d_ws, 0, 16, stream);
-    k_prep<<<576, 256, 0, stream>>>(cb, enc_w3, enc_b3, dec_w1, dec_w2, dec_w3,
-                                    enc_w2, enc_w1,
-                                    P, M, t0, v, csc, cbW, Qbf, w2bf, w3bf,
-                                    Mhi, Mlo, w2ehi, w2elo, w1ehi, w1elo);
-    k_encvq<<<NSAMP / 64, 256, 0, stream>>>(state, enc_w1, enc_b1, enc_w2, enc_b2,
-                                            w1ehi, w1elo, w2ehi, w2elo,
-                                            M, Qbf, Mhi, Mlo, t0, v, csc, P,
-                                            out + OFF_CODE, loss_acc);
-    k_dec<<<NSAMP / 64, 256, 0, stream>>>(out + OFF_CODE, cb, cbW,
-                                          dec_b1, w2bf, dec_b2, w3bf, dec_b3,
-                                          out, out + OFF_RECON);
+
+    const bool big = (ws_size >= (size_t)121728 * 4);
+    if (big) {
+        float* M   = ws + 39424;
+        float* P   = ws + 55808;
+        ushort_t* Mhi = (ushort_t*)(ws + 72192);
+        ushort_t* Mlo = (ushort_t*)(ws + 80384);
+        float* t0  = ws + 88576;
+        float* v   = ws + 88704;
+        float* csc = ws + 88832;
+        ushort_t* w2ehi = (ushort_t*)(ws + 88960);
+        ushort_t* w2elo = (ushort_t*)(ws + 97152);
+        ushort_t* w1ehi = (ushort_t*)(ws + 105344);
+        ushort_t* w1elo = (ushort_t*)(ws + 113536);
+        k_prep<<<576, 256, 0, stream>>>(cb, enc_w3, enc_b3, dec_w1, dec_w2, dec_w3,
+                                        enc_w2, enc_w1,
+                                        P, M, t0, v, csc, cbW, Qbf, w2bf, w3bf,
+                                        Mhi, Mlo, w2ehi, w2elo, w1ehi, w1elo);
+        k_fused<<<NSAMP / 64, 256, 0, stream>>>(state, enc_w1, enc_b1, enc_w2, enc_b2,
+                                                w1ehi, w1elo, w2ehi, w2elo,
+                                                M, Qbf, Mhi, Mlo, t0, v, csc, P,
+                                                out + OFF_CODE, loss_acc,
+                                                cb, cbW, dec_b1, w2bf, dec_b2, w3bf,
+                                                dec_b3, out, out + OFF_RECON);
+    } else {
+        float* P   = out;
+        float* M   = out + 16384;
+        ushort_t* Mhi = (ushort_t*)(out + 32768);
+        ushort_t* Mlo = (ushort_t*)(out + 40960);
+        float* t0  = out + 49152;
+        float* v   = out + 49280;
+        float* csc = out + 49408;
+        ushort_t* w2ehi = (ushort_t*)(out + 49664);
+        ushort_t* w2elo = (ushort_t*)(out + 57856);
+        ushort_t* w1ehi = (ushort_t*)(out + 66048);
+        ushort_t* w1elo = (ushort_t*)(out + 74240);
+        k_prep<<<576, 256, 0, stream>>>(cb, enc_w3, enc_b3, dec_w1, dec_w2, dec_w3,
+                                        enc_w2, enc_w1,
+                                        P, M, t0, v, csc, cbW, Qbf, w2bf, w3bf,
+                                        Mhi, Mlo, w2ehi, w2elo, w1ehi, w1elo);
+        k_encvq<<<NSAMP / 64, 256, 0, stream>>>(state, enc_w1, enc_b1, enc_w2, enc_b2,
+                                                w1ehi, w1elo, w2ehi, w2elo,
+                                                M, Qbf, Mhi, Mlo, t0, v, csc, P,
+                                                out + OFF_CODE, loss_acc);
+        k_dec<<<NSAMP / 64, 256, 0, stream>>>(out + OFF_CODE, cb, cbW,
+                                              dec_b1, w2bf, dec_b2, w3bf, dec_b3,
+                                              out, out + OFF_RECON);
+    }
     k_loss<<<1, 1, 0, stream>>>(loss_acc, out + OFF_LOSS);
 }
```

New measurement: 288.6 us, median of 2. -18.1%, faster.
